# Kernel tuning notes

Measured on AMD Instinct MI355X. Metric: run time of the kernel, lower is better.

Reference implementation:

```python
import jax, jax.numpy as jnp
import numpy as np
import math

B, S, D, H, C, A, SD, L, STEPS = 128, 256, 1024, 16, 50, 32, 64, 6, 10


def setup_inputs():
    key = jax.random.key(0)
    ks = jax.random.split(key, 16)
    rn = lambda k, sh, std=0.02: jax.random.normal(k, sh, jnp.float32) * std
    z = lambda sh: jnp.zeros(sh, jnp.float32)
    o = lambda sh: jnp.ones(sh, jnp.float32)
    return dict(
        reasoning=jax.random.normal(ks[0], (B, S, D), jnp.float32),
        state=jax.random.normal(ks[1], (B, SD), jnp.float32),
        x0=jax.random.normal(ks[2], (B, C, A), jnp.float32),
        W_se=rn(ks[3], (SD, D)), b_se=z(D), g_se=o(D), be_se=z(D),
        W_ap=rn(ks[4], (A, D)), b_ap=z(D),
        W_ad=rn(ks[5], (D, A), 0.001), b_ad=z(A),
        mem_latent=rn(ks[6], (1, 1, D)),
        Wq=rn(ks[7], (D, D)), bq=z(D), Wk=rn(ks[8], (D, D)), bk=z(D),
        Wv=rn(ks[9], (D, D)), bv=z(D), Wo=rn(ks[10], (D, D)), bo=z(D),
        g_q=o(D), be_q=z(D), g_kv=o(D), be_kv=z(D),
        W_fp=rn(ks[11], (D, D)), b_fp=z(D),
        pos_emb=rn(ks[12], (C, D)),
        filmW=rn(ks[13], (L, D, D)), filmb=z((L, D)), filmg=o((L, D)), filmbe=z((L, D)),
        filmWf=rn(ks[14], (L, D, 2 * D)), filmbf=z((L, 2 * D)),
        flow_steps=STEPS,
    )


def _ln(x, g, b):
    m = x.mean(-1, keepdims=True)
    v = jnp.mean((x - m) ** 2, -1, keepdims=True)
    return (x - m) * jax.lax.rsqrt(v + 1e-5) * g + b


def reference(reasoning, state, x0, W_se, b_se, g_se, be_se, W_ap, b_ap, W_ad, b_ad,
              mem_latent, Wq, bq, Wk, bk, Wv, bv, Wo, bo, g_q, be_q, g_kv, be_kv,
              W_fp, b_fp, pos_emb, filmW, filmb, filmg, filmbe, filmWf, filmbf, flow_steps):
    B_, C_, A_ = x0.shape
    D_ = W_ap.shape[1]
    dh = D_ // H
    # --- generate_mem: cross-attn from learned latent over [reasoning; state_enc] ---
    se = _ln(state @ W_se + b_se, g_se, be_se)[:, None, :]          # [B,1,D]
    kv = _ln(jnp.concatenate([reasoning, se], 1), g_kv, be_kv)      # [B,S+1,D]
    q = _ln(jnp.broadcast_to(mem_latent, (B_, 1, D_)), g_q, be_q)   # [B,1,D]
    qh = (q @ Wq + bq).reshape(B_, 1, H, dh)
    kh = (kv @ Wk + bk).reshape(B_, -1, H, dh)
    vh = (kv @ Wv + bv).reshape(B_, -1, H, dh)
    att = jax.nn.softmax(jnp.einsum('bqhd,bkhd->bhqk', qh, kh) / math.sqrt(dh), -1)
    mem = jnp.einsum('bhqk,bkhd->bqhd', att, vh).reshape(B_, 1, D_) @ Wo + bo
    film_vec = mem[:, 0] @ W_fp + b_fp                               # [B,D]
    cond = jnp.broadcast_to(film_vec[:, None, :], (B_, C_, D_)).reshape(B_ * C_, D_)
    half = D_ // 2
    freqs = jnp.exp(jnp.linspace(0.0, math.log(1000.0), half))

    def velocity(x_t, t):
        x = x_t @ W_ap + b_ap + pos_emb[None]                        # [B,C,D]
        targ = t[:, None] * freqs[None, :]
        temb = jnp.concatenate([jnp.sin(targ), jnp.cos(targ)], -1)   # [B,D]
        h = (x + temb[:, None, :]).reshape(B_ * C_, D_)

        def film_step(h, p):
            W, b, g, be, Wf, bf = p
            hh = _ln(h @ W + b, g, be)
            gamma, beta = jnp.split(cond @ Wf + bf, 2, -1)
            return jax.nn.gelu((1.0 + gamma) * hh + beta, approximate=False), None

        h, _ = jax.lax.scan(film_step, h, (filmW, filmb, filmg, filmbe, filmWf, filmbf))
        return (h @ W_ad + b_ad).reshape(B_, C_, A_)

    # --- flow-matching Euler integration (sample) ---
    dt = 1.0 / flow_steps
    ts = jnp.arange(flow_steps, dtype=jnp.float32) * dt

    def euler(x_t, tval):
        v = velocity(x_t, jnp.full((B_,), tval))
        return x_t + v * dt, None

    x_t, _ = jax.lax.scan(euler, x0, ts)
    return x_t
```

## Files before the change

kernel.cpp:

```cpp
#include <hip/hip_runtime.h>
#include <math.h>

#define NB 128
#define NS 256
#define ND 1024
#define NH 16
#define NC 50
#define NA 32
#define NSD 64
#define NL 6
#define NSTEPS 10
#define NM (NB*NC)
#define NKV (NS+1)

typedef unsigned short u16;
typedef short bf16x8 __attribute__((ext_vector_type(8)));
typedef float f32x4 __attribute__((ext_vector_type(4)));
typedef unsigned short us4 __attribute__((ext_vector_type(4)));
typedef unsigned short us8 __attribute__((ext_vector_type(8)));

typedef __attribute__((address_space(1))) const void* gas_p;
typedef __attribute__((address_space(3))) void* las_p;

__device__ __forceinline__ float b2f(u16 h) { return __uint_as_float(((unsigned int)h) << 16); }
__device__ __forceinline__ u16 f2b(float f) {
  unsigned int u = __float_as_uint(f);
  return (u16)((u + 0x7fffu + ((u >> 16) & 1u)) >> 16);
}
__device__ __forceinline__ void gld16(const void* g, void* l) {
  __builtin_amdgcn_global_load_lds((gas_p)g, (las_p)l, 16, 0, 0);
}

__device__ __forceinline__ float wredsum(float v) {
#pragma unroll
  for (int o = 32; o > 0; o >>= 1) v += __shfl_down(v, o, 64);
  return v;
}
__device__ __forceinline__ void bsum2(float& a, float& b, float* red, int t) {
  float ra = wredsum(a), rb = wredsum(b);
  if ((t & 63) == 0) { red[(t >> 6) * 2] = ra; red[(t >> 6) * 2 + 1] = rb; }
  __syncthreads();
  a = red[0] + red[2] + red[4] + red[6];
  b = red[1] + red[3] + red[5] + red[7];
  __syncthreads();
}

__global__ __launch_bounds__(512) void film_gemm(const u16* __restrict__ Ag,
                                                 const u16* __restrict__ Bg,
                                                 u16* __restrict__ Ug) {
  __shared__ u16 As[2][8192];
  __shared__ u16 Bs[2][8192];
  const int t = threadIdx.x, lane = t & 63, w = t >> 6;
  const int rb_ = blockIdx.x;
  const int bid = (rb_ & 7) * 50 + (rb_ >> 3);
  const int tm = bid >> 3, tn = bid & 7;
  const u16* Ab = Ag + (size_t)tm * 128 * ND;
  const u16* Bb = Bg + (size_t)tn * 128 * ND;
  const int c0 = t, c1 = t + 512;
  const int sr0 = c0 >> 3, sq0 = (c0 & 7) ^ (sr0 & 7);
  const int sr1 = c1 >> 3, sq1 = (c1 & 7) ^ (sr1 & 7);
  const int wm = w >> 2, wn = w & 3;
  const int wr = wm * 64, wc = wn * 32;
  const int fr = lane & 15, f8 = lane >> 4, r7 = fr & 7;

  f32x4 acc[4][2];
#pragma unroll
  for (int m = 0; m < 4; ++m)
#pragma unroll
    for (int n = 0; n < 2; ++n)
#pragma unroll
      for (int j = 0; j < 4; ++j) acc[m][n][j] = 0.f;

#define STAGE_FG(buf, k0)                                              \
  gld16(Ab + (size_t)sr0 * ND + (k0) + sq0 * 8, As[buf] + w * 512);    \
  gld16(Ab + (size_t)sr1 * ND + (k0) + sq1 * 8, As[buf] + 4096 + w * 512); \
  gld16(Bb + (size_t)sr0 * ND + (k0) + sq0 * 8, Bs[buf] + w * 512);    \
  gld16(Bb + (size_t)sr1 * ND + (k0) + sq1 * 8, Bs[buf] + 4096 + w * 512);

  STAGE_FG(0, 0)
  __syncthreads();

  for (int it = 0; it < 16; ++it) {
    const int cur = it & 1;
    if (it < 15) { STAGE_FG(cur ^ 1, (it + 1) * 64) }
#pragma unroll
    for (int ks = 0; ks < 2; ++ks) {
      const int qp = (ks * 4 + f8);
      bf16x8 af[4], bfv[2];
#pragma unroll
      for (int m = 0; m < 4; ++m) {
        const int row = wr + m * 16 + fr;
        af[m] = *(const bf16x8*)(As[cur] + row * 64 + (qp ^ r7) * 8);
      }
#pragma unroll
      for (int n = 0; n < 2; ++n) {
        const int row = wc + n * 16 + fr;
        bfv[n] = *(const bf16x8*)(Bs[cur] + row * 64 + (qp ^ r7) * 8);
      }
#pragma unroll
      for (int m = 0; m < 4; ++m)
#pragma unroll
        for (int n = 0; n < 2; ++n)
          acc[m][n] = __builtin_amdgcn_mfma_f32_16x16x32_bf16(af[m], bfv[n], acc[m][n], 0, 0, 0);
    }
    __syncthreads();
  }
#undef STAGE_FG
  u16* Cs = &As[0][0];
#pragma unroll
  for (int m = 0; m < 4; ++m)
#pragma unroll
    for (int n = 0; n < 2; ++n)
#pragma unroll
      for (int j = 0; j < 4; ++j)
        Cs[(wr + m * 16 + f8 * 4 + j) * 128 + wc + n * 16 + fr] = f2b(acc[m][n][j]);
  __syncthreads();
  {
    const int row = t >> 2, cb0 = (t & 3) * 32;
    u16* dst = Ug + (size_t)(tm * 128 + row) * ND + tn * 128 + cb0;
    const u16* srcl = Cs + row * 128 + cb0;
#pragma unroll
    for (int i = 0; i < 4; ++i) *(us8*)(dst + i * 8) = *(const us8*)(srcl + i * 8);
  }
}

__global__ __launch_bounds__(256) void bgemm(const u16* __restrict__ A, const int a_rstride,
    const int a_zoff, const u16* __restrict__ Bp, const long long b_zoff,
    const float* __restrict__ bias, const int bias_zoff, u16* __restrict__ C,
    const int c_rstride, const long long c_zoff) {
  __shared__ u16 As[4096];
  __shared__ u16 Bs[2048];
  const int t = threadIdx.x, wv = t >> 6, lane = t & 63;
  const int nt = blockIdx.x, z = blockIdx.y;
  const u16* Ab = A + (size_t)z * a_zoff;
  const u16* Bb = Bp + (size_t)z * b_zoff + (size_t)nt * 64 * ND;
  const int ca = wv * 128 + lane;
  const int ra0 = ca >> 2, qa0 = (ca & 3) * 8;
  const int ca1 = ca + 64;
  const int ra1 = ca1 >> 2, qa1 = (ca1 & 3) * 8;
  const int cbk = wv * 64 + lane;
  const int rb0 = cbk >> 2, qb0 = (cbk & 3) * 8;
  const int wr = (wv >> 1) * 64, wc = (wv & 1) * 32;
  const int fr = lane & 15, fq = (lane >> 4) * 8;

  f32x4 acc[4][2];
#pragma unroll
  for (int m = 0; m < 4; ++m)
#pragma unroll
    for (int n = 0; n < 2; ++n)
#pragma unroll
      for (int j = 0; j < 4; ++j) acc[m][n][j] = 0.f;

  for (int k0 = 0; k0 < ND; k0 += 32) {
    __syncthreads();
    gld16(Ab + (size_t)ra0 * a_rstride + k0 + qa0, As + wv * 1024);
    gld16(Ab + (size_t)ra1 * a_rstride + k0 + qa1, As + wv * 1024 + 512);
    gld16(Bb + (size_t)rb0 * ND + k0 + qb0, Bs + wv * 512);
    __syncthreads();
    bf16x8 af[4], bfv[2];
#pragma unroll
    for (int m = 0; m < 4; ++m) af[m] = *(const bf16x8*)(As + (wr + m * 16 + fr) * 32 + fq);
#pragma unroll
    for (int n = 0; n < 2; ++n) bfv[n] = *(const bf16x8*)(Bs + (wc + n * 16 + fr) * 32 + fq);
#pragma unroll
    for (int m = 0; m < 4; ++m)
#pragma unroll
      for (int n = 0; n < 2; ++n)
        acc[m][n] = __builtin_amdgcn_mfma_f32_16x16x32_bf16(af[m], bfv[n], acc[m][n], 0, 0, 0);
  }
  const int rb = wr + (lane >> 4) * 4;
#pragma unroll
  for (int n = 0; n < 2; ++n) {
    const int col = nt * 64 + wc + n * 16 + fr;
    const float bz = bias[(size_t)z * bias_zoff + col];
#pragma unroll
    for (int m = 0; m < 4; ++m)
#pragma unroll
      for (int j = 0; j < 4; ++j)
        C[(size_t)z * c_zoff + (size_t)(rb + m * 16 + j) * c_rstride + col] =
            f2b(acc[m][n][j] + bz);
  }
}

__global__ __launch_bounds__(256) void ln_film(const u16* __restrict__ U,
    const float* __restrict__ lb, const float* __restrict__ lg, const float* __restrict__ lbe,
    const u16* __restrict__ gbB, u16* __restrict__ Hout) {
  const int t = threadIdx.x, wv = t >> 6, lane = t & 63;
  const int row = blockIdx.x * 4 + wv;
  const int b = row / NC;
  const int d0 = lane * 16;
  const u16* up = U + (size_t)row * ND + d0;
  us8 u0 = *(const us8*)up;
  us8 u1 = *(const us8*)(up + 8);
  float lbv[16], lgv[16], lbev[16];
#pragma unroll
  for (int i = 0; i < 4; ++i) {
    *(f32x4*)&lbv[i * 4]  = *(const f32x4*)&lb[d0 + i * 4];
    *(f32x4*)&lgv[i * 4]  = *(const f32x4*)&lg[d0 + i * 4];
    *(f32x4*)&lbev[i * 4] = *(const f32x4*)&lbe[d0 + i * 4];
  }
  float x[16];
#pragma unroll
  for (int i = 0; i < 8; ++i) x[i] = b2f((u16)u0[i]) + lbv[i];
#pragma unroll
  for (int i = 0; i < 8; ++i) x[8 + i] = b2f((u16)u1[i]) + lbv[8 + i];
  float s = 0.f, q = 0.f;
#pragma unroll
  for (int i = 0; i < 16; ++i) { s += x[i]; q += x[i] * x[i]; }
#pragma unroll
  for (int o = 32; o > 0; o >>= 1) { s += __shfl_xor(s, o, 64); q += __shfl_xor(q, o, 64); }
  const float m = s * (1.f / ND);
  const float rstd = rsqrtf(q * (1.f / ND) - m * m + 1e-5f);
  const u16* gbb = gbB + (size_t)b * (2 * ND);
  us8 g0 = *(const us8*)(gbb + d0);
  us8 g1 = *(const us8*)(gbb + d0 + 8);
  us8 e0 = *(const us8*)(gbb + ND + d0);
  us8 e1 = *(const us8*)(gbb + ND + d0 + 8);
  us8 o0, o1;
#pragma unroll
  for (int i = 0; i < 16; ++i) {
    const float hh = (x[i] - m) * rstd * lgv[i] + lbev[i];
    const float ga = (i < 8) ? b2f((u16)g0[i]) : b2f((u16)g1[i - 8]);
    const float be = (i < 8) ? b2f((u16)e0[i]) : b2f((u16)e1[i - 8]);
    const float y = (1.f + ga) * hh + be;
    const float gl = 0.5f * y * (1.f + erff(y * 0.70710678118654752f));
    const u16 r = f2b(gl);
    if (i < 8) o0[i] = r; else o1[i - 8] = r;
  }
  u16* op = Hout + (size_t)row * ND + d0;
  *(us8*)op = o0;
  *(us8*)(op + 8) = o1;
}

__global__ __launch_bounds__(256) void h0_mfma(const float* __restrict__ X,
    const u16* __restrict__ WapP, const float* __restrict__ bt,
    const float* __restrict__ pos, u16* __restrict__ Hout) {
  __shared__ u16 As[4096];
  __shared__ u16 Bs[4096];
  const int t = threadIdx.x, wv = t >> 6, lane = t & 63;
  const int r0 = blockIdx.x * 128, c0 = blockIdx.y * 128;
  {
    const int r = t >> 1, hh = (t & 1) * 16;
    const float* xp = X + (size_t)(r0 + r) * NA + hh;
    u16* ad = As + r * 32 + hh;
#pragma unroll
    for (int i = 0; i < 4; ++i) {
      const f32x4 v = *(const f32x4*)(xp + i * 4);
      us4 o;
#pragma unroll
      for (int j = 0; j < 4; ++j) o[j] = f2b(v[j]);
      *(us4*)(ad + i * 4) = o;
    }
  }
  const u16* Bb = WapP + (size_t)c0 * NA;
  {
    const int c = wv * 128 + lane;
    gld16(Bb + (size_t)(c >> 2) * NA + (c & 3) * 8, Bs + wv * 1024);
    const int c1 = c + 64;
    gld16(Bb + (size_t)(c1 >> 2) * NA + (c1 & 3) * 8, Bs + wv * 1024 + 512);
  }
  __syncthreads();
  const int wr = (wv >> 1) * 64, wc = (wv & 1) * 64;
  const int fr = lane & 15, fq = (lane >> 4) * 8;
  bf16x8 af[4], bfv[4];
#pragma unroll
  for (int m = 0; m < 4; ++m) af[m] = *(const bf16x8*)(As + (wr + m * 16 + fr) * 32 + fq);
#pragma unroll
  for (int n = 0; n < 4; ++n) bfv[n] = *(const bf16x8*)(Bs + (wc + n * 16 + fr) * 32 + fq);
  f32x4 acc[4][4];
#pragma unroll
  for (int m = 0; m < 4; ++m)
#pragma unroll
    for (int n = 0; n < 4; ++n) {
#pragma unroll
      for (int j = 0; j < 4; ++j) acc[m][n][j] = 0.f;
      acc[m][n] = __builtin_amdgcn_mfma_f32_16x16x32_bf16(af[m], bfv[n], acc[m][n], 0, 0, 0);
    }
#pragma unroll
  for (int n = 0; n < 4; ++n) {
    const int col = c0 + wc + n * 16 + fr;
    const float btv = bt[col];
#pragma unroll
    for (int m = 0; m < 4; ++m)
#pragma unroll
      for (int j = 0; j < 4; ++j) {
        const int gr = r0 + wr + m * 16 + (lane >> 4) * 4 + j;
        const int c = gr % NC;
        Hout[(size_t)gr * ND + col] = f2b(acc[m][n][j] + btv + pos[(size_t)c * ND + col]);
      }
  }
}

__global__ __launch_bounds__(256) void vx_kernel(const u16* __restrict__ Hf,
    const u16* __restrict__ WadP, const float* __restrict__ b_ad,
    const float* __restrict__ Xin, float* __restrict__ Xout) {
  const int t = threadIdx.x, wv = t >> 6, lane = t & 63;
  const int r0 = blockIdx.x * 64 + wv * 16;
  f32x4 a0, a1;
#pragma unroll
  for (int j = 0; j < 4; ++j) { a0[j] = 0.f; a1[j] = 0.f; }
  const u16* ap = Hf + (size_t)(r0 + (lane & 15)) * ND + (lane >> 4) * 8;
  const u16* bp = WadP + lane * 8;
#pragma unroll 4
  for (int kt = 0; kt < 32; ++kt) {
    bf16x8 av = *(const bf16x8*)(ap + kt * 32);
    bf16x8 w0 = *(const bf16x8*)(bp + (kt * 2 + 0) * 512);
    bf16x8 w1 = *(const bf16x8*)(bp + (kt * 2 + 1) * 512);
    a0 = __builtin_amdgcn_mfma_f32_16x16x32_bf16(av, w0, a0, 0, 0, 0);
    a1 = __builtin_amdgcn_mfma_f32_16x16x32_bf16(av, w1, a1, 0, 0, 0);
  }
  const int rr = r0 + (lane >> 4) * 4;
  const int c0 = lane & 15;
#pragma unroll
  for (int j = 0; j < 4; ++j) {
    const int row = rr + j;
    const int i0 = row * NA + c0;
    Xout[i0] = Xin[i0] + 0.1f * (a0[j] + b_ad[c0]);
    const int i1 = row * NA + 16 + c0;
    Xout[i1] = Xin[i1] + 0.1f * (a1[j] + b_ad[16 + c0]);
  }
}

__global__ __launch_bounds__(256) void packT(const float* __restrict__ src,
    const long long src_zoff, const int srcw, u16* __restrict__ dst,
    const long long dst_zoff) {
  __shared__ float tl[64 * 65];
  const int l = blockIdx.z, kt = blockIdx.y, nt = blockIdx.x;
  const int t = threadIdx.x;
  const float* s = src + (size_t)l * src_zoff + (size_t)(kt * 64) * srcw + nt * 64;
#pragma unroll
  for (int j = 0; j < 4; ++j) {
    const int f = (t + j * 256) * 4;
    const int r = f >> 6, c = f & 63;
    const f32x4 v = *(const f32x4*)&s[(size_t)r * srcw + c];
#pragma unroll
    for (int i = 0; i < 4; ++i) tl[r * 65 + c + i] = v[i];
  }
  __syncthreads();
  const int nn = t >> 2, kg = (t & 3) * 16;
  us8 o0, o1;
#pragma unroll
  for (int i = 0; i < 8; ++i) o0[i] = f2b(tl[(kg + i) * 65 + nn]);
#pragma unroll
  for (int i = 0; i < 8; ++i) o1[i] = f2b(tl[(kg + 8 + i) * 65 + nn]);
  u16* d = dst + (size_t)l * dst_zoff + (size_t)(nt * 64 + nn) * ND + kt * 64 + kg;
  *(us8*)d = o0;
  *(us8*)(d + 8) = o1;
}

__global__ __launch_bounds__(256) void prep_misc(const float* __restrict__ W_ap,
    const float* __restrict__ W_ad, u16* __restrict__ WapP, u16* __restrict__ WadP,
    const float* __restrict__ b_ap, float* __restrict__ bt) {
  const int id = blockIdx.x * 256 + threadIdx.x;
#pragma unroll
  for (int i = 0; i < 4; ++i) {
    const int e = id * 4 + i;
    const int n = e >> 5, k = e & 31;
    WapP[e] = f2b(W_ap[k * ND + n]);
  }
#pragma unroll
  for (int i = 0; i < 4; ++i) {
    const int e = id * 4 + i;
    const int kt = e >> 10, rem = e & 1023;
    const int at = rem >> 9, rem2 = rem & 511;
    const int ln = rem2 >> 3, j = rem2 & 7;
    const int k = kt * 32 + (ln >> 4) * 8 + j;
    const int col = at * 16 + (ln & 15);
    WadP[e] = f2b(W_ad[k * NA + col]);
  }
  if (id < 2560) {
#pragma unroll
    for (int i = 0; i < 4; ++i) {
      const int e = id * 4 + i;
      const int s = e >> 10, d = e & 1023;
      const double lam = 6.907755278982137 / 511.0;
      const double tt = 0.1 * (double)s;
      double v;
      if (d < 512) v = sin(tt * exp(lam * (double)d));
      else         v = cos(tt * exp(lam * (double)(d - 512)));
      bt[e] = (float)v + b_ap[d];
    }
  }
}

__global__ __launch_bounds__(256) void se_kernel(const float* __restrict__ state,
    const float* __restrict__ W_se, const float* __restrict__ b_se,
    const float* __restrict__ g_se, const float* __restrict__ be_se,
    float* __restrict__ se_d) {
  __shared__ float xs[NSD];
  __shared__ float red[8];
  const int b = blockIdx.x, t = threadIdx.x;
  if (t < NSD) xs[t] = state[b * NSD + t];
  __syncthreads();
  const int d0 = t * 4;
  float acc[4];
#pragma unroll
  for (int i = 0; i < 4; ++i) acc[i] = b_se[d0 + i];
  for (int k = 0; k < NSD; ++k) {
    const float xv = xs[k];
    const f32x4 wv = *(const f32x4*)&W_se[(size_t)k * ND + d0];
#pragma unroll
    for (int i = 0; i < 4; ++i) acc[i] += xv * wv[i];
  }
  float s = acc[0] + acc[1] + acc[2] + acc[3];
  float q = acc[0]*acc[0] + acc[1]*acc[1] + acc[2]*acc[2] + acc[3]*acc[3];
  bsum2(s, q, red, t);
  const float m = s * (1.f / ND);
  const float rstd = rsqrtf(q * (1.f / ND) - m * m + 1e-5f);
#pragma unroll
  for (int i = 0; i < 4; ++i)
    se_d[(size_t)b * ND + d0 + i] = (acc[i] - m) * rstd * g_se[d0 + i] + be_se[d0 + i];
}

__global__ __launch_bounds__(256) void q1_kernel(const float* __restrict__ lat,
    const float* __restrict__ g_q, const float* __restrict__ be_q, float* __restrict__ qn) {
  __shared__ float red[8];
  const int t = threadIdx.x;
  const int d0 = t * 4;
  const f32x4 x = *(const f32x4*)&lat[d0];
  float s = x[0] + x[1] + x[2] + x[3];
  float q = x[0]*x[0] + x[1]*x[1] + x[2]*x[2] + x[3]*x[3];
  bsum2(s, q, red, t);
  const float m = s * (1.f / ND);
  const float rstd = rsqrtf(q * (1.f / ND) - m * m + 1e-5f);
#pragma unroll
  for (int i = 0; i < 4; ++i)
    qn[d0 + i] = (x[i] - m) * rstd * g_q[d0 + i] + be_q[d0 + i];
}

__global__ __launch_bounds__(256) void q2_split(const float* __restrict__ qn,
    const float* __restrict__ Wq, float* __restrict__ part) {
  __shared__ float ql[64];
  const int cc = blockIdx.x, kc = blockIdx.y, t = threadIdx.x;
  if (t < 64) ql[t] = qn[kc * 64 + t];
  __syncthreads();
  const int c = cc * 256 + t;
  float acc = 0.f;
#pragma unroll 8
  for (int k = 0; k < 64; ++k) acc += ql[k] * Wq[(size_t)(kc * 64 + k) * ND + c];
  part[kc * ND + c] = acc;
}
__global__ __launch_bounds__(256) void q2_red(const float* __restrict__ part,
    const float* __restrict__ bq, float* __restrict__ qh) {
  const int c = blockIdx.x * 256 + threadIdx.x;
  float a = bq[c];
#pragma unroll
  for (int i = 0; i < 16; ++i) a += part[i * ND + c];
  qh[c] = a;
}

__global__ __launch_bounds__(256) void q3_kernel(const float* __restrict__ Wk,
    const float* __restrict__ bk, const float* __restrict__ qh,
    float* __restrict__ wTf, float* __restrict__ sb) {
  __shared__ float ql[ND];
  __shared__ float wl[4 * ND];
  const int t = threadIdx.x;
  *(f32x4*)&ql[t * 4] = *(const f32x4*)&qh[t * 4];
  const int d0 = blockIdx.x * 4;
  const float* src = Wk + (size_t)d0 * ND;
#pragma unroll
  for (int i = 0; i < 4; ++i)
    *(f32x4*)&wl[(i * 256 + t) * 4] = *(const f32x4*)&src[(size_t)(i * 256 + t) * 4];
  __syncthreads();
  if (t < 64) {
    const int dl = t >> 4, h = t & 15;
    const float* wr_ = wl + dl * ND + h * 64;
    const float* qr = ql + h * 64;
    float acc = 0.f;
#pragma unroll 8
    for (int j = 0; j < 64; ++j) acc += wr_[j] * qr[j];
    wTf[h * ND + d0 + dl] = acc * 0.125f;
  } else if (blockIdx.x == 0 && t >= 64 && t < 80) {
    const int h = t - 64;
    float sv = 0.f;
    for (int j = 0; j < 64; ++j) sv += bk[h * 64 + j] * ql[h * 64 + j];
    sb[h] = sv * 0.125f;
  }
}

__global__ __launch_bounds__(256) void q4_kernel(const float* __restrict__ wTf,
    const float* __restrict__ g_kv, const float* __restrict__ be_kv,
    const float* __restrict__ sb, u16* __restrict__ gwP, float* __restrict__ cgw,
    float* __restrict__ cbw) {
  __shared__ float red[8];
  const int h = blockIdx.x, t = threadIdx.x;
  float pg = 0.f, pb = 0.f;
  for (int d = t; d < ND; d += 256) {
    const float w = wTf[h * ND + d];
    const float gw = g_kv[d] * w;
    gwP[(d >> 5) * 512 + (h + 16 * ((d >> 3) & 3)) * 8 + (d & 7)] = f2b(gw);
    pg += gw;
    pb += be_kv[d] * w;
  }
  bsum2(pg, pb, red, t);
  if (t == 0) { cgw[h] = pg; cbw[h] = pb + sb[h]; }
}

__global__ __launch_bounds__(256) void scores3(const float* __restrict__ reasoning,
    const float* __restrict__ se_d, const u16* __restrict__ gwP,
    const float* __restrict__ cgw, const float* __restrict__ cbw,
    float* __restrict__ scores, float* __restrict__ stats) {
  __shared__ u16 gwl[16384];
  __shared__ float smv[4][16], srv[4][16];
  const int t = threadIdx.x, wv = t >> 6, lane = t & 63;
#pragma unroll
  for (int i = 0; i < 8; ++i)
    gld16(gwP + (i * 256 + t) * 8, gwl + i * 2048 + wv * 512);
  const int r0 = blockIdx.x * 64 + wv * 16;
  const int rowA = r0 + (lane & 15);
  const unsigned bA = (unsigned)rowA / NKV;
  const int kA = rowA - bA * NKV;
  const float* ptr = ((kA < NS) ? reasoning + ((size_t)bA * NS + kA) * ND
                                : se_d + (size_t)bA * ND) + (lane >> 4) * 8;
  __syncthreads();
  f32x4 acc;
#pragma unroll
  for (int j = 0; j < 4; ++j) acc[j] = 0.f;
  float s = 0.f, q = 0.f;
  for (int kt = 0; kt < 32; ++kt) {
    const f32x4 v0 = *(const f32x4*)(ptr + kt * 32);
    const f32x4 v1 = *(const f32x4*)(ptr + kt * 32 + 4);
    bf16x8 af;
#pragma unroll
    for (int j = 0; j < 4; ++j) {
      af[j] = (short)f2b(v0[j]);
      af[4 + j] = (short)f2b(v1[j]);
      s += v0[j] + v1[j];
      q += v0[j] * v0[j] + v1[j] * v1[j];
    }
    const bf16x8 bfr = *(const bf16x8*)(gwl + kt * 512 + lane * 8);
    acc = __builtin_amdgcn_mfma_f32_16x16x32_bf16(af, bfr, acc, 0, 0, 0);
  }
  s += __shfl_xor(s, 16, 64); s += __shfl_xor(s, 32, 64);
  q += __shfl_xor(q, 16, 64); q += __shfl_xor(q, 32, 64);
  const float m = s * (1.f / ND);
  const float rstd = rsqrtf(q * (1.f / ND) - m * m + 1e-5f);
  if (lane < 16) {
    smv[wv][lane] = m; srv[wv][lane] = rstd;
    const int row = r0 + lane;
    stats[(size_t)row * 2] = m;
    stats[(size_t)row * 2 + 1] = rstd;
  }
  __syncthreads();
  const int h = lane & 15;
  const float cg = cgw[h], cb = cbw[h];
#pragma unroll
  for (int j = 0; j < 4; ++j) {
    const int lr = (lane >> 4) * 4 + j;
    const int row = r0 + lr;
    const float mm = smv[wv][lr], rr = srv[wv][lr];
    const unsigned b = (unsigned)row / NKV;
    const int k = row - b * NKV;
    scores[((size_t)b * NH + h) * NKV + k] = rr * acc[j] - rr * mm * cg + cb;
  }
}

__global__ __launch_bounds__(256) void ctx2(const float* __restrict__ reasoning,
    const float* __restrict__ se_d, const float* __restrict__ scores,
    const float* __restrict__ stats, const float* __restrict__ g_kv,
    const float* __restrict__ be_kv, u16* __restrict__ ctxb) {
  __shared__ float sc[NH][260];
  __shared__ float stm[NKV], str[NKV];
  __shared__ float c1s[NH];
  const int chunk = blockIdx.x, b = blockIdx.y;
  const int t = threadIdx.x, wv = t >> 6, lane = t & 63;
#pragma unroll
  for (int h = 0; h < NH; ++h)
    for (int k = t; k < NKV; k += 256) sc[h][k] = scores[((size_t)b * NH + h) * NKV + k];
  for (int k = t; k < NKV; k += 256) {
    stm[k] = stats[((size_t)b * NKV + k) * 2];
    str[k] = stats[((size_t)b * NKV + k) * 2 + 1];
  }
  __syncthreads();
#pragma unroll
  for (int hh = 0; hh < 4; ++hh) {
    const int h = wv * 4 + hh;
    float mx = -1e30f;
    for (int i = 0; i < 5; ++i) { const int k = lane + i * 64; if (k < NKV) mx = fmaxf(mx, sc[h][k]); }
#pragma unroll
    for (int o = 32; o > 0; o >>= 1) mx = fmaxf(mx, __shfl_xor(mx, o, 64));
    float sm = 0.f;
    for (int i = 0; i < 5; ++i) {
      const int k = lane + i * 64;
      if (k < NKV) { const float e = __expf(sc[h][k] - mx); sc[h][k] = e; sm += e; }
    }
#pragma unroll
    for (int o = 32; o > 0; o >>= 1) sm += __shfl_xor(sm, o, 64);
    const float inv = 1.f / sm;
    float c1 = 0.f;
    for (int i = 0; i < 5; ++i) {
      const int k = lane + i * 64;
      if (k < NKV) {
        const float a = sc[h][k] * inv * str[k];
        sc[h][k] = a;
        c1 += a * stm[k];
      }
    }
#pragma unroll
    for (int o = 32; o > 0; o >>= 1) c1 += __shfl_xor(c1, o, 64);
    if (lane == 0) c1s[h] = c1;
  }
  __syncthreads();
  const int c = chunk * 256 + t;
  const float g = g_kv[c], be = be_kv[c];
  float acc[16];
#pragma unroll
  for (int h = 0; h < 16; ++h) acc[h] = 0.f;
  const float* xc = reasoning + (size_t)b * NS * ND + c;
#pragma unroll 2
  for (int k4 = 0; k4 < 64; ++k4) {
    const float x0 = xc[(size_t)(k4 * 4 + 0) * ND];
    const float x1 = xc[(size_t)(k4 * 4 + 1) * ND];
    const float x2 = xc[(size_t)(k4 * 4 + 2) * ND];
    const float x3 = xc[(size_t)(k4 * 4 + 3) * ND];
#pragma unroll
    for (int h = 0; h < 16; ++h) {
      const f32x4 w = *(const f32x4*)&sc[h][k4 * 4];
      acc[h] += w[0] * x0 + w[1] * x1 + w[2] * x2 + w[3] * x3;
    }
  }
  {
    const float xs = se_d[(size_t)b * ND + c];
#pragma unroll
    for (int h = 0; h < 16; ++h) acc[h] += sc[h][NS] * xs;
  }
#pragma unroll
  for (int h = 0; h < 16; ++h)
    ctxb[((size_t)b * NH + h) * ND + c] = f2b(g * (acc[h] - c1s[h]) + be);
}

extern "C" void kernel_launch(void* const* d_in, const int* in_sizes, int n_in,
                              void* d_out, int out_size, void* d_ws, size_t ws_size,
                              hipStream_t stream) {
  (void)in_sizes; (void)n_in; (void)out_size; (void)ws_size;
  const float* reasoning = (const float*)d_in[0];
  const float* state  = (const float*)d_in[1];
  const float* x0     = (const float*)d_in[2];
  const float* W_se   = (const float*)d_in[3];
  const float* b_se   = (const float*)d_in[4];
  const float* g_se   = (const float*)d_in[5];
  const float* be_se  = (const float*)d_in[6];
  const float* W_ap   = (const float*)d_in[7];
  const float* b_ap   = (const float*)d_in[8];
  const float* W_ad   = (const float*)d_in[9];
  const float* b_ad   = (const float*)d_in[10];
  const float* mem_latent = (const float*)d_in[11];
  const float* Wq = (const float*)d_in[12]; const float* bq = (const float*)d_in[13];
  const float* Wk = (const float*)d_in[14]; const float* bk = (const float*)d_in[15];
  const float* Wv = (const float*)d_in[16]; const float* bv = (const float*)d_in[17];
  const float* Wo = (const float*)d_in[18]; const float* bo = (const float*)d_in[19];
  const float* g_q  = (const float*)d_in[20]; const float* be_q  = (const float*)d_in[21];
  const float* g_kv = (const float*)d_in[22]; const float* be_kv = (const float*)d_in[23];
  const float* W_fp = (const float*)d_in[24]; const float* b_fp = (const float*)d_in[25];
  const float* pos_emb = (const float*)d_in[26];
  const float* filmW  = (const float*)d_in[27]; const float* filmb  = (const float*)d_in[28];
  const float* filmg  = (const float*)d_in[29]; const float* filmbe = (const float*)d_in[30];
  const float* filmWf = (const float*)d_in[31]; const float* filmbf = (const float*)d_in[32];

  char* base = (char*)d_ws;
  size_t off = 0;
  auto alloc = [&](size_t bytes) -> void* {
    void* p = base + off;
    off += (bytes + 255) & ~(size_t)255;
    return p;
  };
  u16*  Wpack   = (u16*)alloc((size_t)NL * ND * ND * 2);
  u16*  Wfp2    = (u16*)alloc((size_t)NL * 2 * ND * ND * 2);
  u16*  Wvp     = (u16*)alloc((size_t)ND * ND * 2);
  u16*  Wop     = (u16*)alloc((size_t)ND * ND * 2);
  u16*  Wfpp    = (u16*)alloc((size_t)ND * ND * 2);
  u16*  WapP    = (u16*)alloc((size_t)NA * ND * 2);
  u16*  WadP    = (u16*)alloc((size_t)32768 * 2);
  float* bt     = (float*)alloc((size_t)NSTEPS * ND * 4);
  float* se_d   = (float*)alloc((size_t)NB * ND * 4);
  float* qn     = (float*)alloc((size_t)ND * 4);
  float* qh     = (float*)alloc((size_t)ND * 4);
  float* part   = (float*)alloc((size_t)16 * ND * 4);
  float* wTf    = (float*)alloc((size_t)NH * ND * 4);
  float* sb     = (float*)alloc((size_t)NH * 4);
  u16*  gwP     = (u16*)alloc((size_t)NH * ND * 2);
  float* cgw    = (float*)alloc((size_t)NH * 4);
  float* cbw    = (float*)alloc((size_t)NH * 4);
  float* stats  = (float*)alloc((size_t)NB * NKV * 2 * 4);
  float* scores = (float*)alloc((size_t)NB * NH * NKV * 4);
  u16*  ctxb    = (u16*)alloc((size_t)NB * NH * ND * 2);
  u16*  mem_pre = (u16*)alloc((size_t)NB * ND * 2);
  u16*  memb    = (u16*)alloc((size_t)NB * ND * 2);
  u16*  fvb     = (u16*)alloc((size_t)NB * ND * 2);
  u16*  gbB     = (u16*)alloc((size_t)NL * NB * 2 * ND * 2);
  u16*  hbuf    = (u16*)alloc((size_t)NM * ND * 2);
  u16*  ubuf    = (u16*)alloc((size_t)NM * ND * 2);

  packT<<<dim3(16, 16, NL), 256, 0, stream>>>(filmW, (long long)ND * ND, ND, Wpack,
                                              (long long)ND * ND);
  packT<<<dim3(32, 16, NL), 256, 0, stream>>>(filmWf, (long long)ND * 2 * ND, 2 * ND, Wfp2,
                                              (long long)2 * ND * ND);
  packT<<<dim3(16, 16, 1), 256, 0, stream>>>(Wv, 0, ND, Wvp, 0);
  packT<<<dim3(16, 16, 1), 256, 0, stream>>>(Wo, 0, ND, Wop, 0);
  packT<<<dim3(16, 16, 1), 256, 0, stream>>>(W_fp, 0, ND, Wfpp, 0);
  prep_misc<<<32, 256, 0, stream>>>(W_ap, W_ad, WapP, WadP, b_ap, bt);

  se_kernel<<<NB, 256, 0, stream>>>(state, W_se, b_se, g_se, be_se, se_d);
  q1_kernel<<<1, 256, 0, stream>>>(mem_latent, g_q, be_q, qn);
  q2_split<<<dim3(4, 16), 256, 0, stream>>>(qn, Wq, part);
  q2_red<<<4, 256, 0, stream>>>(part, bq, qh);
  q3_kernel<<<256, 256, 0, stream>>>(Wk, bk, qh, wTf, sb);
  q4_kernel<<<NH, 256, 0, stream>>>(wTf, g_kv, be_kv, sb, gwP, cgw, cbw);
  scores3<<<(NB * NKV) / 64, 256, 0, stream>>>(reasoning, se_d, gwP, cgw, cbw, scores, stats);
  ctx2<<<dim3(4, NB), 256, 0, stream>>>(reasoning, se_d, scores, stats, g_kv, be_kv, ctxb);
  bgemm<<<dim3(1, 16), 256, 0, stream>>>(ctxb, NH * ND, ND, Wvp, (long long)64 * ND, bv, 64,
                                         mem_pre, ND, 64);
  bgemm<<<dim3(16, 1), 256, 0, stream>>>(mem_pre, ND, 0, Wop, 0, bo, 0, memb, ND, 0);
  bgemm<<<dim3(16, 1), 256, 0, stream>>>(memb, ND, 0, Wfpp, 0, b_fp, 0, fvb, ND, 0);
  bgemm<<<dim3(32, NL), 256, 0, stream>>>(fvb, ND, 0, Wfp2, (long long)2 * ND * ND, filmbf,
                                          2 * ND, gbB, 2 * ND, (long long)NB * 2 * ND);

  for (int s = 0; s < NSTEPS; ++s) {
    const float* xin = (s == 0) ? x0 : (const float*)d_out;
    h0_mfma<<<dim3(NM / 128, 8), 256, 0, stream>>>(xin, WapP, bt + (size_t)s * ND, pos_emb,
                                                   hbuf);
    for (int l = 0; l < NL; ++l) {
      film_gemm<<<400, 512, 0, stream>>>(hbuf, Wpack + (size_t)l * ND * ND, ubuf);
      ln_film<<<NM / 4, 256, 0, stream>>>(ubuf, filmb + (size_t)l * ND, filmg + (size_t)l * ND,
                                          filmbe + (size_t)l * ND,
                                          gbB + (size_t)l * NB * 2 * ND, hbuf);
    }
    vx_kernel<<<NM / 64, 256, 0, stream>>>(hbuf, WadP, b_ad, xin, (float*)d_out);
  }
}
```

Baseline: 2.590 ms.

## Split K across wave groups in film_gemm with shared-memory reduction

Result: faster. 2.517 ms (-2.8%).

```diff
diff --git a/kernel.cpp b/kernel.cpp
--- a/kernel.cpp
+++ b/kernel.cpp
@@ -48,8 +48,8 @@
 __global__ __launch_bounds__(512) void film_gemm(const u16* __restrict__ Ag,
                                                  const u16* __restrict__ Bg,
                                                  u16* __restrict__ Ug) {
-  __shared__ u16 As[2][8192];
-  __shared__ u16 Bs[2][8192];
+  __shared__ __align__(16) char smemc[65536];
+  u16* smemu = (u16*)smemc;
   const int t = threadIdx.x, lane = t & 63, w = t >> 6;
   const int rb_ = blockIdx.x;
   const int bid = (rb_ & 7) * 50 + (rb_ >> 3);
@@ -59,61 +59,86 @@
   const int c0 = t, c1 = t + 512;
   const int sr0 = c0 >> 3, sq0 = (c0 & 7) ^ (sr0 & 7);
   const int sr1 = c1 >> 3, sq1 = (c1 & 7) ^ (sr1 & 7);
-  const int wm = w >> 2, wn = w & 3;
-  const int wr = wm * 64, wc = wn * 32;
+  const int wq = w & 3, ksel = w >> 2;
+  const int wr = (wq >> 1) * 64, wc = (wq & 1) * 64;
   const int fr = lane & 15, f8 = lane >> 4, r7 = fr & 7;
-
-  f32x4 acc[4][2];
+  const int qp = ksel * 4 + f8;
+
+  f32x4 acc[4][4];
 #pragma unroll
   for (int m = 0; m < 4; ++m)
 #pragma unroll
-    for (int n = 0; n < 2; ++n)
+    for (int n = 0; n < 4; ++n)
 #pragma unroll
       for (int j = 0; j < 4; ++j) acc[m][n][j] = 0.f;
 
-#define STAGE_FG(buf, k0)                                              \
-  gld16(Ab + (size_t)sr0 * ND + (k0) + sq0 * 8, As[buf] + w * 512);    \
-  gld16(Ab + (size_t)sr1 * ND + (k0) + sq1 * 8, As[buf] + 4096 + w * 512); \
-  gld16(Bb + (size_t)sr0 * ND + (k0) + sq0 * 8, Bs[buf] + w * 512);    \
-  gld16(Bb + (size_t)sr1 * ND + (k0) + sq1 * 8, Bs[buf] + 4096 + w * 512);
+#define STAGE_FG(bofs, k0)                                                      \
+  gld16(Ab + (size_t)sr0 * ND + (k0) + sq0 * 8, smemu + (bofs) + w * 512 + lane * 8 - lane * 8); \
+  gld16(Ab + (size_t)sr1 * ND + (k0) + sq1 * 8, smemu + (bofs) + 4096 + w * 512);               \
+  gld16(Bb + (size_t)sr0 * ND + (k0) + sq0 * 8, smemu + 16384 + (bofs) + w * 512);              \
+  gld16(Bb + (size_t)sr1 * ND + (k0) + sq1 * 8, smemu + 16384 + (bofs) + 4096 + w * 512);
 
   STAGE_FG(0, 0)
   __syncthreads();
 
   for (int it = 0; it < 16; ++it) {
-    const int cur = it & 1;
-    if (it < 15) { STAGE_FG(cur ^ 1, (it + 1) * 64) }
-#pragma unroll
-    for (int ks = 0; ks < 2; ++ks) {
-      const int qp = (ks * 4 + f8);
-      bf16x8 af[4], bfv[2];
-#pragma unroll
-      for (int m = 0; m < 4; ++m) {
-        const int row = wr + m * 16 + fr;
-        af[m] = *(const bf16x8*)(As[cur] + row * 64 + (qp ^ r7) * 8);
-      }
-#pragma unroll
-      for (int n = 0; n < 2; ++n) {
-        const int row = wc + n * 16 + fr;
-        bfv[n] = *(const bf16x8*)(Bs[cur] + row * 64 + (qp ^ r7) * 8);
-      }
-#pragma unroll
-      for (int m = 0; m < 4; ++m)
-#pragma unroll
-        for (int n = 0; n < 2; ++n)
-          acc[m][n] = __builtin_amdgcn_mfma_f32_16x16x32_bf16(af[m], bfv[n], acc[m][n], 0, 0, 0);
-    }
+    const int bofs = (it & 1) * 8192;
+    if (it < 15) { STAGE_FG(8192 - bofs, (it + 1) * 64) }
+    const u16* Asc = smemu + bofs;
+    const u16* Bsc = smemu + 16384 + bofs;
+    bf16x8 af[4], bfv[4];
+#pragma unroll
+    for (int m = 0; m < 4; ++m) {
+      const int row = wr + m * 16 + fr;
+      af[m] = *(const bf16x8*)(Asc + row * 64 + (qp ^ r7) * 8);
+    }
+#pragma unroll
+    for (int n = 0; n < 4; ++n) {
+      const int row = wc + n * 16 + fr;
+      bfv[n] = *(const bf16x8*)(Bsc + row * 64 + (qp ^ r7) * 8);
+    }
+#pragma unroll
+    for (int m = 0; m < 4; ++m)
+#pragma unroll
+      for (int n = 0; n < 4; ++n)
+        acc[m][n] = __builtin_amdgcn_mfma_f32_16x16x32_bf16(af[m], bfv[n], acc[m][n], 0, 0, 0);
     __syncthreads();
   }
 #undef STAGE_FG
-  u16* Cs = &As[0][0];
-#pragma unroll
-  for (int m = 0; m < 4; ++m)
-#pragma unroll
-    for (int n = 0; n < 2; ++n)
-#pragma unroll
-      for (int j = 0; j < 4; ++j)
-        Cs[(wr + m * 16 + f8 * 4 + j) * 128 + wc + n * 16 + fr] = f2b(acc[m][n][j]);
+
+  float* Cred = (float*)smemc;
+  if (w >= 4) {
+    const int base = (w - 4) * 4096;
+#pragma unroll
+    for (int m = 0; m < 4; ++m)
+#pragma unroll
+      for (int n = 0; n < 4; ++n)
+#pragma unroll
+        for (int j = 0; j < 4; ++j)
+          Cred[base + (m * 16 + f8 * 4 + j) * 64 + n * 16 + fr] = acc[m][n][j];
+  }
+  __syncthreads();
+  if (w < 4) {
+    const int base = w * 4096;
+#pragma unroll
+    for (int m = 0; m < 4; ++m)
+#pragma unroll
+      for (int n = 0; n < 4; ++n)
+#pragma unroll
+        for (int j = 0; j < 4; ++j)
+          acc[m][n][j] += Cred[base + (m * 16 + f8 * 4 + j) * 64 + n * 16 + fr];
+  }
+  __syncthreads();
+  u16* Cs = smemu;
+  if (w < 4) {
+#pragma unroll
+    for (int m = 0; m < 4; ++m)
+#pragma unroll
+      for (int n = 0; n < 4; ++n)
+#pragma unroll
+        for (int j = 0; j < 4; ++j)
+          Cs[(wr + m * 16 + f8 * 4 + j) * 128 + wc + n * 16 + fr] = f2b(acc[m][n][j]);
+  }
   __syncthreads();
   {
     const int row = t >> 2, cb0 = (t & 3) * 32;
```

## Prepack FiLM weights into MFMA fragment order and load B directly to registers

Applied to the files above, without the earlier changes.

New measurement: 2.627 ms. About the same (+1.4%).

```diff
diff --git a/kernel.cpp b/kernel.cpp
--- a/kernel.cpp
+++ b/kernel.cpp
@@ -46,22 +46,21 @@
 }
 
 __global__ __launch_bounds__(512) void film_gemm(const u16* __restrict__ Ag,
-                                                 const u16* __restrict__ Bg,
+                                                 const u16* __restrict__ Wf,
                                                  u16* __restrict__ Ug) {
-  __shared__ u16 As[2][8192];
-  __shared__ u16 Bs[2][8192];
+  __shared__ __align__(16) u16 smemu[16384];
   const int t = threadIdx.x, lane = t & 63, w = t >> 6;
   const int rb_ = blockIdx.x;
   const int bid = (rb_ & 7) * 50 + (rb_ >> 3);
   const int tm = bid >> 3, tn = bid & 7;
   const u16* Ab = Ag + (size_t)tm * 128 * ND;
-  const u16* Bb = Bg + (size_t)tn * 128 * ND;
-  const int c0 = t, c1 = t + 512;
-  const int sr0 = c0 >> 3, sq0 = (c0 & 7) ^ (sr0 & 7);
+  const int sr0 = t >> 3, sq0 = (t & 7) ^ (sr0 & 7);
+  const int c1 = t + 512;
   const int sr1 = c1 >> 3, sq1 = (c1 & 7) ^ (sr1 & 7);
   const int wm = w >> 2, wn = w & 3;
   const int wr = wm * 64, wc = wn * 32;
   const int fr = lane & 15, f8 = lane >> 4, r7 = fr & 7;
+  const u16* WfB = Wf + ((size_t)(tn * 8 + wn * 2) * 32) * 512 + lane * 8;
 
   f32x4 acc[4][2];
 #pragma unroll
@@ -71,42 +70,42 @@
 #pragma unroll
       for (int j = 0; j < 4; ++j) acc[m][n][j] = 0.f;
 
-#define STAGE_FG(buf, k0)                                              \
-  gld16(Ab + (size_t)sr0 * ND + (k0) + sq0 * 8, As[buf] + w * 512);    \
-  gld16(Ab + (size_t)sr1 * ND + (k0) + sq1 * 8, As[buf] + 4096 + w * 512); \
-  gld16(Bb + (size_t)sr0 * ND + (k0) + sq0 * 8, Bs[buf] + w * 512);    \
-  gld16(Bb + (size_t)sr1 * ND + (k0) + sq1 * 8, Bs[buf] + 4096 + w * 512);
-
-  STAGE_FG(0, 0)
+#define STAGE_A(buf, k0)                                                          \
+  gld16(Ab + (size_t)sr0 * ND + (k0) + sq0 * 8, smemu + (buf) * 8192 + w * 512);  \
+  gld16(Ab + (size_t)sr1 * ND + (k0) + sq1 * 8, smemu + (buf) * 8192 + 4096 + w * 512);
+
+  STAGE_A(0, 0)
   __syncthreads();
 
   for (int it = 0; it < 16; ++it) {
     const int cur = it & 1;
-    if (it < 15) { STAGE_FG(cur ^ 1, (it + 1) * 64) }
+    bf16x8 bAll[2][2];
+#pragma unroll
+    for (int ks = 0; ks < 2; ++ks)
+#pragma unroll
+      for (int n = 0; n < 2; ++n)
+        bAll[ks][n] = *(const bf16x8*)(WfB + ((size_t)n * 32 + it * 2 + ks) * 512);
+    if (it < 15) { STAGE_A(cur ^ 1, (it + 1) * 64) }
+    const u16* Asc = smemu + cur * 8192;
 #pragma unroll
     for (int ks = 0; ks < 2; ++ks) {
-      const int qp = (ks * 4 + f8);
-      bf16x8 af[4], bfv[2];
-#pragma unroll
-      for (int m = 0; m < 4; ++m) {
-        const int row = wr + m * 16 + fr;
-        af[m] = *(const bf16x8*)(As[cur] + row * 64 + (qp ^ r7) * 8);
-      }
-#pragma unroll
-      for (int n = 0; n < 2; ++n) {
-        const int row = wc + n * 16 + fr;
-        bfv[n] = *(const bf16x8*)(Bs[cur] + row * 64 + (qp ^ r7) * 8);
-      }
+      const int qp = ks * 4 + f8;
+      bf16x8 af[4];
 #pragma unroll
       for (int m = 0; m < 4; ++m)
+        af[m] = *(const bf16x8*)(Asc + (wr + m * 16 + fr) * 64 + (qp ^ r7) * 8);
+#pragma unroll
+      for (int m = 0; m < 4; ++m)
 #pragma unroll
         for (int n = 0; n < 2; ++n)
-          acc[m][n] = __builtin_amdgcn_mfma_f32_16x16x32_bf16(af[m], bfv[n], acc[m][n], 0, 0, 0);
+          acc[m][n] = __builtin_amdgcn_mfma_f32_16x16x32_bf16(af[m], bAll[ks][n],
+                                                              acc[m][n], 0, 0, 0);
     }
     __syncthreads();
   }
-#undef STAGE_FG
-  u16* Cs = &As[0][0];
+#undef STAGE_A
+
+  u16* Cs = smemu;
 #pragma unroll
   for (int m = 0; m < 4; ++m)
 #pragma unroll
@@ -122,6 +121,36 @@
 #pragma unroll
     for (int i = 0; i < 4; ++i) *(us8*)(dst + i * 8) = *(const us8*)(srcl + i * 8);
   }
+}
+
+__global__ __launch_bounds__(256) void packF(const float* __restrict__ src,
+                                             u16* __restrict__ dst) {
+  __shared__ float tl[64 * 65];
+  const int l = blockIdx.z, kt64 = blockIdx.y, nt64 = blockIdx.x;
+  const int t = threadIdx.x;
+  const float* s = src + (size_t)l * ND * ND + (size_t)(kt64 * 64) * ND + nt64 * 64;
+#pragma unroll
+  for (int j = 0; j < 4; ++j) {
+    const int f = (t + j * 256) * 4;
+    const int r = f >> 6, c = f & 63;
+    const f32x4 v = *(const f32x4*)&s[(size_t)r * ND + c];
+#pragma unroll
+    for (int i = 0; i < 4; ++i) tl[r * 65 + c + i] = v[i];
+  }
+  __syncthreads();
+  const int nn = t >> 2, kg = (t & 3) * 16;
+  us8 o0, o1;
+#pragma unroll
+  for (int i = 0; i < 8; ++i) o0[i] = f2b(tl[(kg + i) * 65 + nn]);
+#pragma unroll
+  for (int i = 0; i < 8; ++i) o1[i] = f2b(tl[(kg + 8 + i) * 65 + nn]);
+  const int n = nt64 * 64 + nn;
+  const int kbase = kt64 * 64 + kg;
+  u16* base_ = dst + (size_t)l * ND * ND + ((size_t)(n >> 4) * 32 + (kbase >> 5)) * 512;
+  const int lane0 = (n & 15) + 16 * ((kbase >> 3) & 3);
+  const int lane1 = (n & 15) + 16 * (((kbase + 8) >> 3) & 3);
+  *(us8*)(base_ + lane0 * 8) = o0;
+  *(us8*)(base_ + lane1 * 8) = o1;
 }
 
 __global__ __launch_bounds__(256) void bgemm(const u16* __restrict__ A, const int a_rstride,
@@ -237,6 +266,7 @@
     const float* __restrict__ pos, u16* __restrict__ Hout) {
   __shared__ u16 As[4096];
   __shared__ u16 Bs[4096];
+  __shared__ u16 Cs[16384];
   const int t = threadIdx.x, wv = t >> 6, lane = t & 63;
   const int r0 = blockIdx.x * 128, c0 = blockIdx.y * 128;
   {
@@ -284,10 +314,18 @@
     for (int m = 0; m < 4; ++m)
 #pragma unroll
       for (int j = 0; j < 4; ++j) {
-        const int gr = r0 + wr + m * 16 + (lane >> 4) * 4 + j;
-        const int c = gr % NC;
-        Hout[(size_t)gr * ND + col] = f2b(acc[m][n][j] + btv + pos[(size_t)c * ND + col]);
+        const int lr = wr + m * 16 + (lane >> 4) * 4 + j;
+        const int c = (r0 + lr) % NC;
+        Cs[lr * 128 + wc + n * 16 + fr] = f2b(acc[m][n][j] + btv + pos[(size_t)c * ND + col]);
       }
+  }
+  __syncthreads();
+  {
+    const int row = t >> 1, cb0 = (t & 1) * 64;
+    u16* dst = Hout + (size_t)(r0 + row) * ND + c0 + cb0;
+    const u16* srcl = Cs + row * 128 + cb0;
+#pragma unroll
+    for (int i = 0; i < 8; ++i) *(us8*)(dst + i * 8) = *(const us8*)(srcl + i * 8);
   }
 }
 
@@ -664,7 +702,7 @@
     off += (bytes + 255) & ~(size_t)255;
     return p;
   };
-  u16*  Wpack   = (u16*)alloc((size_t)NL * ND * ND * 2);
+  u16*  Wfrag   = (u16*)alloc((size_t)NL * ND * ND * 2);
   u16*  Wfp2    = (u16*)alloc((size_t)NL * 2 * ND * ND * 2);
   u16*  Wvp     = (u16*)alloc((size_t)ND * ND * 2);
   u16*  Wop     = (u16*)alloc((size_t)ND * ND * 2);
@@ -691,8 +729,7 @@
   u16*  hbuf    = (u16*)alloc((size_t)NM * ND * 2);
   u16*  ubuf    = (u16*)alloc((size_t)NM * ND * 2);
 
-  packT<<<dim3(16, 16, NL), 256, 0, stream>>>(filmW, (long long)ND * ND, ND, Wpack,
-                                              (long long)ND * ND);
+  packF<<<dim3(16, 16, NL), 256, 0, stream>>>(filmW, Wfrag);
   packT<<<dim3(32, 16, NL), 256, 0, stream>>>(filmWf, (long long)ND * 2 * ND, 2 * ND, Wfp2,
                                               (long long)2 * ND * ND);
   packT<<<dim3(16, 16, 1), 256, 0, stream>>>(Wv, 0, ND, Wvp, 0);
@@ -720,7 +757,7 @@
     h0_mfma<<<dim3(NM / 128, 8), 256, 0, stream>>>(xin, WapP, bt + (size_t)s * ND, pos_emb,
                                                    hbuf);
     for (int l = 0; l < NL; ++l) {
-      film_gemm<<<400, 512, 0, stream>>>(hbuf, Wpack + (size_t)l * ND * ND, ubuf);
+      film_gemm<<<400, 512, 0, stream>>>(hbuf, Wfrag + (size_t)l * ND * ND, ubuf);
       ln_film<<<NM / 4, 256, 0, stream>>>(ubuf, filmb + (size_t)l * ND, filmg + (size_t)l * ND,
                                           filmbe + (size_t)l * ND,
                                           gbB + (size_t)l * NB * 2 * ND, hbuf);
```
